# Kernel optimization log

Hardware: AMD Instinct MI355X
Metric: run time of the kernel (lower is better)

## Reference

```python
import jax, jax.numpy as jnp
import numpy as np

NB, DIM, DSTATE, DCONV, EXPAND = 4, 256, 16, 4, 2
DIN = EXPAND * DIM                 # 512
DTRANK = (DIM + 15) // 16          # 16, mamba-ssm default dt_rank = ceil(d_model/16)
B, L = 16, 512


def layer_norm(x, w, b, eps=1e-5):
    mu = x.mean(-1, keepdims=True)
    var = x.var(-1, keepdims=True)
    return (x - mu) * jax.lax.rsqrt(var + eps) * w + b


def selective_scan(u, delta, A, Bm, Cm, D):
    # u, delta: (B,L,DIN); Bm,Cm: (B,L,N); A: (DIN,N); D: (DIN,)
    def step(h, xs):
        d_t, B_t, C_t, u_t = xs          # (B,DIN), (B,N), (B,N), (B,DIN)
        dA = jnp.exp(d_t[..., None] * A)                                  # (B,DIN,N)
        h = dA * h + d_t[..., None] * B_t[:, None, :] * u_t[..., None]   # (B,DIN,N)
        y = jnp.einsum('bdn,bn->bd', h, C_t)
        return h, y

    h0 = jnp.zeros((u.shape[0], u.shape[2], A.shape[1]), u.dtype)
    xs = (delta.transpose(1, 0, 2), Bm.transpose(1, 0, 2),
          Cm.transpose(1, 0, 2), u.transpose(1, 0, 2))
    _, ys = jax.lax.scan(step, h0, xs)
    return ys.transpose(1, 0, 2) + u * D


def mamba_block(x, ln_w, ln_b, in_w, in_b, cw, cb, xp_w, dtw, dtb, A_log, D, ow):
    h = layer_norm(x, ln_w, ln_b)
    xz = h @ in_w.T + in_b                       # (B,L,2*DIN)
    xin, z = xz[..., :DIN], xz[..., DIN:]
    # causal depthwise conv over the sequence dim
    xc = jax.lax.conv_general_dilated(
        xin.transpose(0, 2, 1), cw[:, None, :], (1,), [(DCONV - 1, 0)],
        dimension_numbers=('NCH', 'OIH', 'NCH'), feature_group_count=DIN)
    xc = jax.nn.silu(xc + cb[None, :, None]).transpose(0, 2, 1)   # (B,L,DIN)
    dbc = xc @ xp_w.T                                             # (B,L,DTRANK+2*N)
    dt = jax.nn.softplus(dbc[..., :DTRANK] @ dtw.T + dtb)         # (B,L,DIN)
    Bm = dbc[..., DTRANK:DTRANK + DSTATE]
    Cm = dbc[..., DTRANK + DSTATE:]
    y = selective_scan(xc, dt, -jnp.exp(A_log), Bm, Cm, D)
    return x + (y * jax.nn.silu(z)) @ ow.T       # dropout = identity at eval


def setup_inputs() -> dict:
    key = jax.random.key(0)
    ks = jax.random.split(key, 8)
    s = 0.02
    A_log = jnp.tile(jnp.log(jnp.arange(1, DSTATE + 1, dtype=jnp.float32))[None, None, :],
                     (NB, DIN, 1))
    return {
        'x': jax.random.normal(ks[0], (B, L, DIM), jnp.float32),
        'ln_w': jnp.ones((NB, DIM), jnp.float32),
        'ln_b': jnp.zeros((NB, DIM), jnp.float32),
        'in_proj_w': jax.random.normal(ks[1], (NB, 2 * DIN, DIM), jnp.float32) * s,
        'in_proj_b': jnp.zeros((NB, 2 * DIN), jnp.float32),
        'conv_w': jax.random.normal(ks[2], (NB, DIN, DCONV), jnp.float32) * s,
        'conv_b': jnp.zeros((NB, DIN), jnp.float32),
        'x_proj_w': jax.random.normal(ks[3], (NB, DTRANK + 2 * DSTATE, DIN), jnp.float32) * s,
        'dt_proj_w': jax.random.normal(ks[4], (NB, DIN, DTRANK), jnp.float32) * s,
        'dt_proj_b': jax.random.uniform(ks[5], (NB, DIN), jnp.float32, -4.0, -3.0),
        'A_log': A_log,
        'D': jnp.ones((NB, DIN), jnp.float32),
        'out_proj_w': jax.random.normal(ks[6], (NB, DIM, DIN), jnp.float32) * s,
    }


def reference(x, ln_w, ln_b, in_proj_w, in_proj_b, conv_w, conv_b, x_proj_w,
              dt_proj_w, dt_proj_b, A_log, D, out_proj_w):
    for i in range(NB):
        x = mamba_block(x, ln_w[i], ln_b[i], in_proj_w[i], in_proj_b[i],
                        conv_w[i], conv_b[i], x_proj_w[i], dt_proj_w[i],
                        dt_proj_b[i], A_log[i], D[i], out_proj_w[i])
    return x
```

## Files before the change

### kernel.cpp

```cpp
#include <hip/hip_runtime.h>
#include <math.h>

#define NB 4
#define DIMM 256
#define DSTATE 16
#define DCONV 4
#define DIN 512
#define DTRANK 16
#define BB 16
#define LL 512
#define TT (BB * LL)
#define XZ_DIM (2 * DIN)
#define DBC_DIM (DTRANK + 2 * DSTATE)
#define NC 32
#define CHUNK (LL / NC)

__device__ __forceinline__ unsigned short f2bf(float f) {
    union { float f; unsigned int u; } v; v.f = f;
    unsigned int r = v.u + 0x7fff + ((v.u >> 16) & 1);
    return (unsigned short)(r >> 16);
}
__device__ __forceinline__ float bf2f(unsigned short u) {
    union { unsigned int i; float f; } v; v.i = ((unsigned int)u) << 16;
    return v.f;
}

__global__ __launch_bounds__(256) void cvt3_kernel(const float* __restrict__ s1,
                                                   unsigned short* __restrict__ d1, int n1,
                                                   const float* __restrict__ s2,
                                                   unsigned short* __restrict__ d2, int n2,
                                                   const float* __restrict__ s3,
                                                   unsigned short* __restrict__ d3, int n3) {
    int stride = gridDim.x * 256;
    for (int i = blockIdx.x * 256 + threadIdx.x; i < n1; i += stride) {
        float4 v = ((const float4*)s1)[i];
        ushort4 o; o.x = f2bf(v.x); o.y = f2bf(v.y); o.z = f2bf(v.z); o.w = f2bf(v.w);
        ((ushort4*)d1)[i] = o;
    }
    for (int i = blockIdx.x * 256 + threadIdx.x; i < n2; i += stride) {
        float4 v = ((const float4*)s2)[i];
        ushort4 o; o.x = f2bf(v.x); o.y = f2bf(v.y); o.z = f2bf(v.z); o.w = f2bf(v.w);
        ((ushort4*)d2)[i] = o;
    }
    for (int i = blockIdx.x * 256 + threadIdx.x; i < n3; i += stride) {
        float4 v = ((const float4*)s3)[i];
        ushort4 o; o.x = f2bf(v.x); o.y = f2bf(v.y); o.z = f2bf(v.z); o.w = f2bf(v.w);
        ((ushort4*)d3)[i] = o;
    }
}

__global__ __launch_bounds__(256) void ln_kernel(const float* __restrict__ x,
                                                 const float* __restrict__ w,
                                                 const float* __restrict__ bvec,
                                                 unsigned short* __restrict__ out) {
    int t = blockIdx.x;
    int i = threadIdx.x;
    float v = x[t * DIMM + i];
    float s = v, s2 = v * v;
#pragma unroll
    for (int off = 1; off < 64; off <<= 1) {
        s  += __shfl_xor(s, off);
        s2 += __shfl_xor(s2, off);
    }
    __shared__ float ss[4], ss2[4];
    int wid = i >> 6;
    if ((i & 63) == 0) { ss[wid] = s; ss2[wid] = s2; }
    __syncthreads();
    s  = ss[0] + ss[1] + ss[2] + ss[3];
    s2 = ss2[0] + ss2[1] + ss2[2] + ss2[3];
    float mu  = s * (1.0f / DIMM);
    float var = s2 * (1.0f / DIMM) - mu * mu;
    float r   = rsqrtf(var + 1e-5f);
    out[t * DIMM + i] = f2bf((v - mu) * r * w[i] + bvec[i]);
}

#define GBM2 128
#define GBN2 128
#define GBK2 32
#define LDW2 (GBK2 + 8)
__global__ __launch_bounds__(256) void gemm128(const unsigned short* __restrict__ A, int lda,
                                               const unsigned short* __restrict__ Bw, int ldb,
                                               const float* __restrict__ bias,
                                               unsigned short* __restrict__ C1b,
                                               unsigned short* __restrict__ C2b, int nsplit,
                                               int ldc, int K) {
    using short8  = __attribute__((ext_vector_type(8))) short;
    using floatx4 = __attribute__((ext_vector_type(4))) float;
    __shared__ __align__(16) unsigned short As[GBM2 * LDW2];
    __shared__ __align__(16) unsigned short Bs[GBN2 * LDW2];

    int tid  = threadIdx.x;
    int m0   = blockIdx.y * GBM2;
    int n0   = blockIdx.x * GBN2;
    int w    = tid >> 6;
    int lane = tid & 63;
    int wm   = (w & 1) * 64;
    int wn   = (w >> 1) * 64;
    int lr   = lane & 15;
    int quad = lane >> 4;

    floatx4 acc[4][4] = {};

    int ar = tid >> 1;
    int ak = (tid & 1) * 16;

    for (int k0 = 0; k0 < K; k0 += GBK2) {
        {
            const unsigned short* src = &A[(size_t)(m0 + ar) * lda + k0 + ak];
            int4 a0 = *(const int4*)(src);
            int4 a1 = *(const int4*)(src + 8);
            *(int4*)&As[ar * LDW2 + ak]     = a0;
            *(int4*)&As[ar * LDW2 + ak + 8] = a1;
        }
        {
            const unsigned short* src = &Bw[(size_t)(n0 + ar) * ldb + k0 + ak];
            int4 b0 = *(const int4*)(src);
            int4 b1 = *(const int4*)(src + 8);
            *(int4*)&Bs[ar * LDW2 + ak]     = b0;
            *(int4*)&Bs[ar * LDW2 + ak + 8] = b1;
        }
        __syncthreads();
        short8 af[4], bf[4];
#pragma unroll
        for (int i = 0; i < 4; ++i)
            af[i] = *(const short8*)&As[(wm + i * 16 + lr) * LDW2 + quad * 8];
#pragma unroll
        for (int j = 0; j < 4; ++j)
            bf[j] = *(const short8*)&Bs[(wn + j * 16 + lr) * LDW2 + quad * 8];
#pragma unroll
        for (int i = 0; i < 4; ++i)
#pragma unroll
            for (int j = 0; j < 4; ++j)
                acc[i][j] = __builtin_amdgcn_mfma_f32_16x16x32_bf16(af[i], bf[j], acc[i][j], 0, 0, 0);
        __syncthreads();
    }

#pragma unroll
    for (int j = 0; j < 4; ++j) {
        int cn = n0 + wn + j * 16 + lr;
        float bb = bias ? bias[cn] : 0.0f;
        unsigned short* dst = (cn < nsplit) ? C1b : C2b;
        int col = (cn < nsplit) ? cn : cn - nsplit;
#pragma unroll
        for (int i = 0; i < 4; ++i)
#pragma unroll
            for (int r = 0; r < 4; ++r) {
                int cm = m0 + wm + i * 16 + quad * 4 + r;
                dst[(size_t)cm * ldc + col] = f2bf(acc[i][j][r] + bb);
            }
    }
}

#define TBM 128
#define TBN 64
#define TBK 32
#define LDKW (TBK + 8)
__global__ __launch_bounds__(256) void gemm_bf16(const unsigned short* __restrict__ A, int lda,
                                                 const unsigned short* __restrict__ Bw, int ldb,
                                                 const float* __restrict__ bias,
                                                 const float* __restrict__ resid,
                                                 float* __restrict__ C,
                                                 unsigned short* __restrict__ C1b,
                                                 unsigned short* __restrict__ C2b, int nsplit,
                                                 int ldc, int N, int K) {
    using short8  = __attribute__((ext_vector_type(8))) short;
    using floatx4 = __attribute__((ext_vector_type(4))) float;
    __shared__ __align__(16) unsigned short As[TBM * LDKW];
    __shared__ __align__(16) unsigned short Bs[TBN * LDKW];

    int tid  = threadIdx.x;
    int m0   = blockIdx.y * TBM;
    int n0   = blockIdx.x * TBN;
    int w    = tid >> 6;
    int lane = tid & 63;
    int wm   = (w & 1) * 64;
    int wn   = (w >> 1) * 32;
    int lr   = lane & 15;
    int quad = lane >> 4;

    floatx4 acc[4][2] = {};

    int ar = tid >> 1;
    int ak = (tid & 1) * 16;
    int br = tid >> 2;
    int bk = (tid & 3) * 8;

    for (int k0 = 0; k0 < K; k0 += TBK) {
        {
            const unsigned short* src = &A[(size_t)(m0 + ar) * lda + k0 + ak];
            int4 a0 = *(const int4*)(src);
            int4 a1 = *(const int4*)(src + 8);
            *(int4*)&As[ar * LDKW + ak]     = a0;
            *(int4*)&As[ar * LDKW + ak + 8] = a1;
        }
        {
            int gn = n0 + br;
            int4 b0 = make_int4(0, 0, 0, 0);
            if (gn < N) b0 = *(const int4*)&Bw[(size_t)gn * ldb + k0 + bk];
            *(int4*)&Bs[br * LDKW + bk] = b0;
        }
        __syncthreads();
        short8 af[4], bf[2];
#pragma unroll
        for (int i = 0; i < 4; ++i)
            af[i] = *(const short8*)&As[(wm + i * 16 + lr) * LDKW + quad * 8];
#pragma unroll
        for (int j = 0; j < 2; ++j)
            bf[j] = *(const short8*)&Bs[(wn + j * 16 + lr) * LDKW + quad * 8];
#pragma unroll
        for (int i = 0; i < 4; ++i)
#pragma unroll
            for (int j = 0; j < 2; ++j)
                acc[i][j] = __builtin_amdgcn_mfma_f32_16x16x32_bf16(af[i], bf[j], acc[i][j], 0, 0, 0);
        __syncthreads();
    }

#pragma unroll
    for (int j = 0; j < 2; ++j) {
        int cn = n0 + wn + j * 16 + lr;
        if (cn < N) {
            float bb = bias ? bias[cn] : 0.0f;
            if (C1b) {
                unsigned short* dst = (cn < nsplit) ? C1b : C2b;
                int col = (cn < nsplit) ? cn : cn - nsplit;
#pragma unroll
                for (int i = 0; i < 4; ++i)
#pragma unroll
                    for (int r = 0; r < 4; ++r) {
                        int cm = m0 + wm + i * 16 + quad * 4 + r;
                        dst[(size_t)cm * ldc + col] = f2bf(acc[i][j][r] + bb);
                    }
            } else {
#pragma unroll
                for (int i = 0; i < 4; ++i)
#pragma unroll
                    for (int r = 0; r < 4; ++r) {
                        int cm = m0 + wm + i * 16 + quad * 4 + r;
                        float v = acc[i][j][r] + bb;
                        if (resid) v += resid[(size_t)cm * ldc + cn];
                        C[(size_t)cm * ldc + cn] = v;
                    }
            }
        }
    }
}

__global__ __launch_bounds__(256) void conv_silu(const unsigned short* __restrict__ Xb,
                                                 const float* __restrict__ cw,
                                                 const float* __restrict__ cb,
                                                 unsigned short* __restrict__ xcb) {
    int idx = blockIdx.x * blockDim.x + threadIdx.x;
    int d = idx & (DIN - 1);
    int t = idx >> 9;
    int l = t & (LL - 1);
    int bq = t >> 9;
    float acc = cb[d];
#pragma unroll
    for (int k = 0; k < DCONV; ++k) {
        int ls = l - (DCONV - 1) + k;
        if (ls >= 0) acc += cw[d * DCONV + k] * bf2f(Xb[(size_t)(bq * LL + ls) * DIN + d]);
    }
    float v = acc / (1.0f + __expf(-acc));
    xcb[(size_t)t * DIN + d] = f2bf(v);
}

__global__ __launch_bounds__(256) void dt_kernel(const float* __restrict__ dbc,
                                                 const float* __restrict__ dtw,
                                                 const float* __restrict__ dtbias,
                                                 unsigned short* __restrict__ dtout) {
    int idx = blockIdx.x * blockDim.x + threadIdx.x;
    int d = idx & (DIN - 1);
    int t = idx >> 9;
    float a = dtbias[d];
    const float4* wv = (const float4*)(dtw + d * DTRANK);
    const float* dr = dbc + (size_t)t * DBC_DIM;
#pragma unroll
    for (int q = 0; q < 4; ++q) {
        float4 w4 = wv[q];
        a += w4.x * dr[q * 4 + 0] + w4.y * dr[q * 4 + 1] +
             w4.z * dr[q * 4 + 2] + w4.w * dr[q * 4 + 3];
    }
    float sp = (a > 20.0f) ? a : log1pf(__expf(a));
    dtout[(size_t)t * DIN + d] = f2bf(sp);
}

__global__ __launch_bounds__(256) void scan_p1(const unsigned short* __restrict__ xcb,
                                               const unsigned short* __restrict__ dtb,
                                               const float* __restrict__ dbc,
                                               const float* __restrict__ A_log,
                                               float* __restrict__ S,
                                               float* __restrict__ H) {
    int bid = blockIdx.x;
    int dq = bid & 3;
    int c  = (bid >> 2) & (NC - 1);
    int b  = bid >> 7;
    int dloc = threadIdx.x >> 1;
    int sh   = threadIdx.x & 1;
    int d  = dq * 128 + dloc;
    int n0 = sh * 8;
    int base = b * LL + c * CHUNK;

    __shared__ float LB[CHUNK * DBC_DIM];
    for (int i = threadIdx.x; i < CHUNK * DBC_DIM / 4; i += 256)
        ((float4*)LB)[i] = ((const float4*)(dbc + (size_t)base * DBC_DIM))[i];

    float a[8];
    {
        const float4* ar = (const float4*)(A_log + d * DSTATE + n0);
        float4 v0 = ar[0], v1 = ar[1];
        a[0] = -__expf(v0.x); a[1] = -__expf(v0.y); a[2] = -__expf(v0.z); a[3] = -__expf(v0.w);
        a[4] = -__expf(v1.x); a[5] = -__expf(v1.y); a[6] = -__expf(v1.z); a[7] = -__expf(v1.w);
    }
    __syncthreads();

    float h[8];
#pragma unroll
    for (int j = 0; j < 8; ++j) h[j] = 0.0f;
    float Ssum = 0.0f;
    float u   = bf2f(xcb[(size_t)base * DIN + d]);
    float dtv = bf2f(dtb[(size_t)base * DIN + d]);
#pragma unroll 4
    for (int s = 0; s < CHUNK; ++s) {
        float nu  = bf2f(xcb[(size_t)(base + s + 1) * DIN + d]);
        float ndt = bf2f(dtb[(size_t)(base + s + 1) * DIN + d]);
        const float* row = &LB[s * DBC_DIM];
        float4 b0 = *(const float4*)&row[DTRANK + n0];
        float4 b1 = *(const float4*)&row[DTRANK + n0 + 4];
        const float btv[8] = {b0.x, b0.y, b0.z, b0.w, b1.x, b1.y, b1.z, b1.w};
        Ssum += dtv;
        float wv = dtv * u;
#pragma unroll
        for (int j = 0; j < 8; ++j) {
            float dA = __expf(dtv * a[j]);
            h[j] = dA * h[j] + wv * btv[j];
        }
        u = nu; dtv = ndt;
    }
    size_t sc = (size_t)b * NC + c;
    if (sh == 0) S[sc * DIN + d] = Ssum;
#pragma unroll
    for (int j = 0; j < 8; ++j) H[(sc * DIN + d) * 16 + n0 + j] = h[j];
}

__global__ __launch_bounds__(256) void scan_p2(const float* __restrict__ A_log,
                                               const float* __restrict__ S,
                                               float* __restrict__ H) {
    int idx = blockIdx.x * 256 + threadIdx.x;
    int n = idx & 15;
    int d = (idx >> 4) & (DIN - 1);
    int b = idx >> 13;
    float a = -__expf(A_log[d * DSTATE + n]);
    float h = 0.0f;
#pragma unroll
    for (int c = 0; c < NC; ++c) {
        size_t sc = (size_t)b * NC + c;
        float Sv = S[sc * DIN + d];
        size_t q = (sc * DIN + d) * 16 + n;
        float Hc = H[q];
        H[q] = h;
        h = __expf(a * Sv) * h + Hc;
    }
}

__global__ __launch_bounds__(256) void scan_p3(const unsigned short* __restrict__ xcb,
                                               const unsigned short* __restrict__ dtb,
                                               const unsigned short* __restrict__ Zb,
                                               const float* __restrict__ dbc,
                                               const float* __restrict__ A_log,
                                               const float* __restrict__ Dp,
                                               const float* __restrict__ Hin,
                                               unsigned short* __restrict__ gb) {
    int bid = blockIdx.x;
    int dq = bid & 3;
    int c  = (bid >> 2) & (NC - 1);
    int b  = bid >> 7;
    int dloc = threadIdx.x >> 1;
    int sh   = threadIdx.x & 1;
    int d  = dq * 128 + dloc;
    int n0 = sh * 8;
    int base = b * LL + c * CHUNK;

    __shared__ float LB[CHUNK * DBC_DIM];
    for (int i = threadIdx.x; i < CHUNK * DBC_DIM / 4; i += 256)
        ((float4*)LB)[i] = ((const float4*)(dbc + (size_t)base * DBC_DIM))[i];

    float a[8];
    {
        const float4* ar = (const float4*)(A_log + d * DSTATE + n0);
        float4 v0 = ar[0], v1 = ar[1];
        a[0] = -__expf(v0.x); a[1] = -__expf(v0.y); a[2] = -__expf(v0.z); a[3] = -__expf(v0.w);
        a[4] = -__expf(v1.x); a[5] = -__expf(v1.y); a[6] = -__expf(v1.z); a[7] = -__expf(v1.w);
    }
    float Dd = Dp[d];
    size_t sc = (size_t)b * NC + c;
    float h[8];
#pragma unroll
    for (int j = 0; j < 8; ++j) h[j] = Hin[(sc * DIN + d) * 16 + n0 + j];
    __syncthreads();

    float u   = bf2f(xcb[(size_t)base * DIN + d]);
    float dtv = bf2f(dtb[(size_t)base * DIN + d]);
#pragma unroll 4
    for (int s = 0; s < CHUNK; ++s) {
        float nu  = bf2f(xcb[(size_t)(base + s + 1) * DIN + d]);
        float ndt = bf2f(dtb[(size_t)(base + s + 1) * DIN + d]);
        const float* row = &LB[s * DBC_DIM];
        float4 b0 = *(const float4*)&row[DTRANK + n0];
        float4 b1 = *(const float4*)&row[DTRANK + n0 + 4];
        float4 c0 = *(const float4*)&row[DTRANK + DSTATE + n0];
        float4 c1 = *(const float4*)&row[DTRANK + DSTATE + n0 + 4];
        const float btv[8] = {b0.x, b0.y, b0.z, b0.w, b1.x, b1.y, b1.z, b1.w};
        const float ctv[8] = {c0.x, c0.y, c0.z, c0.w, c1.x, c1.y, c1.z, c1.w};
        float wv = dtv * u;
        float y  = (sh == 0) ? u * Dd : 0.0f;
#pragma unroll
        for (int j = 0; j < 8; ++j) {
            float dA = __expf(dtv * a[j]);
            h[j] = dA * h[j] + wv * btv[j];
            y += h[j] * ctv[j];
        }
        y += __shfl_xor(y, 1);
        if (sh == 0) {
            float zf = bf2f(Zb[(size_t)(base + s) * DIN + d]);
            float g = y * (zf / (1.0f + __expf(-zf)));
            gb[(size_t)(base + s) * DIN + d] = f2bf(g);
        }
        u = nu; dtv = ndt;
    }
}

extern "C" void kernel_launch(void* const* d_in, const int* in_sizes, int n_in,
                              void* d_out, int out_size, void* d_ws, size_t ws_size,
                              hipStream_t stream) {
    const float* x_in   = (const float*)d_in[0];
    const float* ln_w   = (const float*)d_in[1];
    const float* ln_b   = (const float*)d_in[2];
    const float* in_w   = (const float*)d_in[3];
    const float* in_b   = (const float*)d_in[4];
    const float* conv_w = (const float*)d_in[5];
    const float* conv_b = (const float*)d_in[6];
    const float* xp_w   = (const float*)d_in[7];
    const float* dt_w   = (const float*)d_in[8];
    const float* dt_b   = (const float*)d_in[9];
    const float* A_log  = (const float*)d_in[10];
    const float* Dp     = (const float*)d_in[11];
    const float* ow     = (const float*)d_in[12];
    float* out = (float*)d_out;

    const size_t M = 1048576;
    float* ws = (float*)d_ws;
    float* xbuf = ws;
    unsigned short* hb  = (unsigned short*)(ws + 2 * M);
    float* dbc = ws + 3 * M;
    unsigned short* Xb  = (unsigned short*)(ws + 4 * M);
    unsigned short* Zb  = (unsigned short*)(ws + 6 * M);
    unsigned short* xcb = (unsigned short*)(ws + 8 * M);
    unsigned short* dtb = (unsigned short*)(ws + 10 * M);
    unsigned short* gb  = (unsigned short*)(ws + 12 * M);
    float* Hbuf = ws + 14 * M;
    float* Sbuf = ws + 18 * M;
    unsigned short* inwb = (unsigned short*)(ws + 18 * M + 262144);
    unsigned short* owb  = inwb + (size_t)NB * XZ_DIM * DIMM;
    unsigned short* xpwb = owb + (size_t)NB * DIMM * DIN;

    cvt3_kernel<<<256, 256, 0, stream>>>(
        in_w, inwb, NB * XZ_DIM * DIMM / 4,
        ow,   owb,  NB * DIMM * DIN / 4,
        xp_w, xpwb, NB * DBC_DIM * DIN / 4);

    for (int layer = 0; layer < NB; ++layer) {
        const float* xi = (layer == 0) ? x_in : xbuf;
        float* xo = (layer == NB - 1) ? out : xbuf;

        ln_kernel<<<TT, 256, 0, stream>>>(xi, ln_w + layer * DIMM, ln_b + layer * DIMM, hb);

        gemm128<<<dim3(XZ_DIM / GBN2, TT / GBM2), 256, 0, stream>>>(
            hb, DIMM, inwb + (size_t)layer * XZ_DIM * DIMM, DIMM,
            in_b + layer * XZ_DIM, Xb, Zb, DIN, DIN, DIMM);

        conv_silu<<<(TT * DIN) / 256, 256, 0, stream>>>(
            Xb, conv_w + layer * DIN * DCONV, conv_b + layer * DIN, xcb);

        gemm_bf16<<<dim3(1, TT / TBM), 256, 0, stream>>>(
            xcb, DIN, xpwb + (size_t)layer * DBC_DIM * DIN, DIN,
            nullptr, nullptr, dbc, nullptr, nullptr, 0, DBC_DIM, DBC_DIM, DIN);

        dt_kernel<<<(TT * DIN) / 256, 256, 0, stream>>>(
            dbc, dt_w + (size_t)layer * DIN * DTRANK, dt_b + layer * DIN, dtb);

        const float* Al = A_log + (size_t)layer * DIN * DSTATE;
        scan_p1<<<BB * NC * 4, 256, 0, stream>>>(xcb, dtb, dbc, Al, Sbuf, Hbuf);
        scan_p2<<<(BB * DIN * 16) / 256, 256, 0, stream>>>(Al, Sbuf, Hbuf);
        scan_p3<<<BB * NC * 4, 256, 0, stream>>>(xcb, dtb, Zb, dbc, Al,
                                                 Dp + layer * DIN, Hbuf, gb);

        gemm_bf16<<<dim3(DIMM / TBN, TT / TBM), 256, 0, stream>>>(
            gb, DIN, owb + (size_t)layer * DIMM * DIN, DIN,
            nullptr, xi, xo, nullptr, nullptr, 0, DIMM, DIMM, DIN);
    }
}
```

Before: 681.8 us.

## Fuse layernorm into in_proj GEMM and conv+x_proj+dt_proj into one kernel

```diff
diff --git a/kernel.cpp b/kernel.cpp
--- a/kernel.cpp
+++ b/kernel.cpp
@@ -49,45 +49,23 @@
     }
 }
 
-__global__ __launch_bounds__(256) void ln_kernel(const float* __restrict__ x,
-                                                 const float* __restrict__ w,
-                                                 const float* __restrict__ bvec,
-                                                 unsigned short* __restrict__ out) {
-    int t = blockIdx.x;
-    int i = threadIdx.x;
-    float v = x[t * DIMM + i];
-    float s = v, s2 = v * v;
-#pragma unroll
-    for (int off = 1; off < 64; off <<= 1) {
-        s  += __shfl_xor(s, off);
-        s2 += __shfl_xor(s2, off);
-    }
-    __shared__ float ss[4], ss2[4];
-    int wid = i >> 6;
-    if ((i & 63) == 0) { ss[wid] = s; ss2[wid] = s2; }
-    __syncthreads();
-    s  = ss[0] + ss[1] + ss[2] + ss[3];
-    s2 = ss2[0] + ss2[1] + ss2[2] + ss2[3];
-    float mu  = s * (1.0f / DIMM);
-    float var = s2 * (1.0f / DIMM) - mu * mu;
-    float r   = rsqrtf(var + 1e-5f);
-    out[t * DIMM + i] = f2bf((v - mu) * r * w[i] + bvec[i]);
-}
-
 #define GBM2 128
 #define GBN2 128
 #define GBK2 32
 #define LDW2 (GBK2 + 8)
-__global__ __launch_bounds__(256) void gemm128(const unsigned short* __restrict__ A, int lda,
-                                               const unsigned short* __restrict__ Bw, int ldb,
-                                               const float* __restrict__ bias,
-                                               unsigned short* __restrict__ C1b,
-                                               unsigned short* __restrict__ C2b, int nsplit,
-                                               int ldc, int K) {
+__global__ __launch_bounds__(256) void ln_inproj(const float* __restrict__ x,
+                                                 const float* __restrict__ lnw,
+                                                 const float* __restrict__ lnb,
+                                                 const unsigned short* __restrict__ Bw,
+                                                 const float* __restrict__ bias,
+                                                 unsigned short* __restrict__ C1b,
+                                                 unsigned short* __restrict__ C2b,
+                                                 int nsplit, int ldc) {
     using short8  = __attribute__((ext_vector_type(8))) short;
     using floatx4 = __attribute__((ext_vector_type(4))) float;
     __shared__ __align__(16) unsigned short As[GBM2 * LDW2];
     __shared__ __align__(16) unsigned short Bs[GBN2 * LDW2];
+    __shared__ float muS[GBM2], rsS[GBM2], lwS[DIMM], lbS[DIMM];
 
     int tid  = threadIdx.x;
     int m0   = blockIdx.y * GBM2;
@@ -99,21 +77,54 @@
     int lr   = lane & 15;
     int quad = lane >> 4;
 
+    {
+        int r = tid >> 1;
+        int seg = (tid & 1) * 128;
+        const float4* xr = (const float4*)(x + (size_t)(m0 + r) * DIMM + seg);
+        float s = 0.0f, s2 = 0.0f;
+#pragma unroll
+        for (int i = 0; i < 32; ++i) {
+            float4 v = xr[i];
+            s  += v.x + v.y + v.z + v.w;
+            s2 += v.x * v.x + v.y * v.y + v.z * v.z + v.w * v.w;
+        }
+        s  += __shfl_xor(s, 1);
+        s2 += __shfl_xor(s2, 1);
+        if ((tid & 1) == 0) {
+            float mu  = s * (1.0f / DIMM);
+            float var = s2 * (1.0f / DIMM) - mu * mu;
+            muS[r] = mu;
+            rsS[r] = rsqrtf(var + 1e-5f);
+        }
+        lwS[tid] = lnw[tid];
+        lbS[tid] = lnb[tid];
+    }
+    __syncthreads();
+
     floatx4 acc[4][4] = {};
 
     int ar = tid >> 1;
     int ak = (tid & 1) * 16;
 
-    for (int k0 = 0; k0 < K; k0 += GBK2) {
+    for (int k0 = 0; k0 < DIMM; k0 += GBK2) {
         {
-            const unsigned short* src = &A[(size_t)(m0 + ar) * lda + k0 + ak];
-            int4 a0 = *(const int4*)(src);
-            int4 a1 = *(const int4*)(src + 8);
-            *(int4*)&As[ar * LDW2 + ak]     = a0;
-            *(int4*)&As[ar * LDW2 + ak + 8] = a1;
+            float mu = muS[ar], rs = rsS[ar];
+            const float4* src = (const float4*)(x + (size_t)(m0 + ar) * DIMM + k0 + ak);
+            unsigned short tmp[16];
+#pragma unroll
+            for (int q = 0; q < 4; ++q) {
+                float4 v = src[q];
+                int kk = k0 + ak + q * 4;
+                tmp[q * 4 + 0] = f2bf((v.x - mu) * rs * lwS[kk + 0] + lbS[kk + 0]);
+                tmp[q * 4 + 1] = f2bf((v.y - mu) * rs * lwS[kk + 1] + lbS[kk + 1]);
+                tmp[q * 4 + 2] = f2bf((v.z - mu) * rs * lwS[kk + 2] + lbS[kk + 2]);
+                tmp[q * 4 + 3] = f2bf((v.w - mu) * rs * lwS[kk + 3] + lbS[kk + 3]);
+            }
+            *(int4*)&As[ar * LDW2 + ak]     = *(const int4*)&tmp[0];
+            *(int4*)&As[ar * LDW2 + ak + 8] = *(const int4*)&tmp[8];
         }
         {
-            const unsigned short* src = &Bw[(size_t)(n0 + ar) * ldb + k0 + ak];
+            const unsigned short* src = &Bw[(size_t)(n0 + ar) * DIMM + k0 + ak];
             int4 b0 = *(const int4*)(src);
             int4 b1 = *(const int4*)(src + 8);
             *(int4*)&Bs[ar * LDW2 + ak]     = b0;
@@ -138,7 +149,7 @@
 #pragma unroll
     for (int j = 0; j < 4; ++j) {
         int cn = n0 + wn + j * 16 + lr;
-        float bb = bias ? bias[cn] : 0.0f;
+        float bb = bias[cn];
         unsigned short* dst = (cn < nsplit) ? C1b : C2b;
         int col = (cn < nsplit) ? cn : cn - nsplit;
 #pragma unroll
@@ -148,6 +159,115 @@
                 int cm = m0 + wm + i * 16 + quad * 4 + r;
                 dst[(size_t)cm * ldc + col] = f2bf(acc[i][j][r] + bb);
             }
+    }
+}
+
+#define CXM 64
+__global__ __launch_bounds__(256) void conv_xp(const unsigned short* __restrict__ Xb,
+                                               const float* __restrict__ cw,
+                                               const float* __restrict__ cb,
+                                               const unsigned short* __restrict__ xpw,
+                                               const float* __restrict__ dtw,
+                                               const float* __restrict__ dtbias,
+                                               unsigned short* __restrict__ xcb,
+                                               float* __restrict__ dbc,
+                                               unsigned short* __restrict__ dtout) {
+    using short8  = __attribute__((ext_vector_type(8))) short;
+    using floatx4 = __attribute__((ext_vector_type(4))) float;
+    __shared__ __align__(16) unsigned short As[CXM * LDW2];
+    __shared__ __align__(16) unsigned short Bs[48 * LDW2];
+    __shared__ float dbcS[CXM * DBC_DIM];
+
+    int t0 = blockIdx.x * CXM;
+    int bq = t0 >> 9;
+    int l0 = t0 & (LL - 1);
+    int tid  = threadIdx.x;
+    int w    = tid >> 6;
+    int lane = tid & 63;
+    int lr   = lane & 15;
+    int quad = lane >> 4;
+    int wm   = w * 16;
+
+    int ch = tid & 31;
+    int tg = tid >> 5;
+    int br = tid >> 2;
+    int bk = (tid & 3) * 8;
+
+    floatx4 acc[3] = {};
+
+    for (int k0 = 0; k0 < DIN; k0 += 32) {
+        int d = k0 + ch;
+        float4 cwv = *(const float4*)&cw[d * DCONV];
+        float cbv = cb[d];
+        const float cwk[4] = {cwv.x, cwv.y, cwv.z, cwv.w};
+#pragma unroll
+        for (int tt = 0; tt < 8; ++tt) {
+            int l = l0 + tg * 8 + tt;
+            int t = t0 + tg * 8 + tt;
+            float a0 = cbv;
+#pragma unroll
+            for (int k = 0; k < DCONV; ++k) {
+                int ls = l - (DCONV - 1) + k;
+                if (ls >= 0) a0 += cwk[k] * bf2f(Xb[(size_t)(bq * LL + ls) * DIN + d]);
+            }
+            float v = a0 / (1.0f + __expf(-a0));
+            unsigned short bv = f2bf(v);
+            As[(tg * 8 + tt) * LDW2 + ch] = bv;
+            xcb[(size_t)t * DIN + d] = bv;
+        }
+        if (br < 48) {
+            int4 b0 = *(const int4*)&xpw[(size_t)br * DIN + k0 + bk];
+            *(int4*)&Bs[br * LDW2 + bk] = b0;
+        }
+        __syncthreads();
+        short8 af = *(const short8*)&As[(wm + lr) * LDW2 + quad * 8];
+#pragma unroll
+        for (int j = 0; j < 3; ++j) {
+            short8 bf = *(const short8*)&Bs[(j * 16 + lr) * LDW2 + quad * 8];
+            acc[j] = __builtin_amdgcn_mfma_f32_16x16x32_bf16(af, bf, acc[j], 0, 0, 0);
+        }
+        __syncthreads();
+    }
+
+#pragma unroll
+    for (int j = 0; j < 3; ++j) {
+        int col = j * 16 + lr;
+#pragma unroll
+        for (int r = 0; r < 4; ++r) {
+            int row = wm + quad * 4 + r;
+            float v = acc[j][r];
+            dbcS[row * DBC_DIM + col] = v;
+            dbc[(size_t)(t0 + row) * DBC_DIM + col] = v;
+        }
+    }
+    __syncthreads();
+
+    {
+        int d0 = tid * 2;
+        float wa[16], wb[16];
+        const float4* wra = (const float4*)(dtw + d0 * DTRANK);
+        const float4* wrb = (const float4*)(dtw + (d0 + 1) * DTRANK);
+#pragma unroll
+        for (int q = 0; q < 4; ++q) {
+            float4 va = wra[q], vb = wrb[q];
+            wa[q * 4 + 0] = va.x; wa[q * 4 + 1] = va.y; wa[q * 4 + 2] = va.z; wa[q * 4 + 3] = va.w;
+            wb[q * 4 + 0] = vb.x; wb[q * 4 + 1] = vb.y; wb[q * 4 + 2] = vb.z; wb[q * 4 + 3] = vb.w;
+        }
+        float ba = dtbias[d0], bb = dtbias[d0 + 1];
+        for (int tt = 0; tt < CXM; ++tt) {
+            const float* row = &dbcS[tt * DBC_DIM];
+            float da = ba, db = bb;
+#pragma unroll
+            for (int q = 0; q < 4; ++q) {
+                float4 rv = *(const float4*)&row[q * 4];
+                da += rv.x * wa[q*4+0] + rv.y * wa[q*4+1] + rv.z * wa[q*4+2] + rv.w * wa[q*4+3];
+                db += rv.x * wb[q*4+0] + rv.y * wb[q*4+1] + rv.z * wb[q*4+2] + rv.w * wb[q*4+3];
+            }
+            float sa = (da > 20.0f) ? da : log1pf(__expf(da));
+            float sb = (db > 20.0f) ? db : log1pf(__expf(db));
+            unsigned int packed = (unsigned int)f2bf(sa) | ((unsigned int)f2bf(sb) << 16);
+            *(unsigned int*)&dtout[(size_t)(t0 + tt) * DIN + d0] = packed;
+        }
     }
 }
 
@@ -243,45 +363,6 @@
             }
         }
     }
-}
-
-__global__ __launch_bounds__(256) void conv_silu(const unsigned short* __restrict__ Xb,
-                                                 const float* __restrict__ cw,
-                                                 const float* __restrict__ cb,
-                                                 unsigned short* __restrict__ xcb) {
-    int idx = blockIdx.x * blockDim.x + threadIdx.x;
-    int d = idx & (DIN - 1);
-    int t = idx >> 9;
-    int l = t & (LL - 1);
-    int bq = t >> 9;
-    float acc = cb[d];
-#pragma unroll
-    for (int k = 0; k < DCONV; ++k) {
-        int ls = l - (DCONV - 1) + k;
-        if (ls >= 0) acc += cw[d * DCONV + k] * bf2f(Xb[(size_t)(bq * LL + ls) * DIN + d]);
-    }
-    float v = acc / (1.0f + __expf(-acc));
-    xcb[(size_t)t * DIN + d] = f2bf(v);
-}
-
-__global__ __launch_bounds__(256) void dt_kernel(const float* __restrict__ dbc,
-                                                 const float* __restrict__ dtw,
-                                                 const float* __restrict__ dtbias,
-                                                 unsigned short* __restrict__ dtout) {
-    int idx = blockIdx.x * blockDim.x + threadIdx.x;
-    int d = idx & (DIN - 1);
-    int t = idx >> 9;
-    float a = dtbias[d];
-    const float4* wv = (const float4*)(dtw + d * DTRANK);
-    const float* dr = dbc + (size_t)t * DBC_DIM;
-#pragma unroll
-    for (int q = 0; q < 4; ++q) {
-        float4 w4 = wv[q];
-        a += w4.x * dr[q * 4 + 0] + w4.y * dr[q * 4 + 1] +
-             w4.z * dr[q * 4 + 2] + w4.w * dr[q * 4 + 3];
-    }
-    float sp = (a > 20.0f) ? a : log1pf(__expf(a));
-    dtout[(size_t)t * DIN + d] = f2bf(sp);
 }
 
 __global__ __launch_bounds__(256) void scan_p1(const unsigned short* __restrict__ xcb,
@@ -450,7 +531,6 @@
     const size_t M = 1048576;
     float* ws = (float*)d_ws;
     float* xbuf = ws;
-    unsigned short* hb  = (unsigned short*)(ws + 2 * M);
     float* dbc = ws + 3 * M;
     unsigned short* Xb  = (unsigned short*)(ws + 4 * M);
     unsigned short* Zb  = (unsigned short*)(ws + 6 * M);
@@ -472,21 +552,16 @@
         const float* xi = (layer == 0) ? x_in : xbuf;
         float* xo = (layer == NB - 1) ? out : xbuf;
 
-        ln_kernel<<<TT, 256, 0, stream>>>(xi, ln_w + layer * DIMM, ln_b + layer * DIMM, hb);
-
-        gemm128<<<dim3(XZ_DIM / GBN2, TT / GBM2), 256, 0, stream>>>(
-            hb, DIMM, inwb + (size_t)layer * XZ_DIM * DIMM, DIMM,
-            in_b + layer * XZ_DIM, Xb, Zb, DIN, DIN, DIMM);
-
-        conv_silu<<<(TT * DIN) / 256, 256, 0, stream>>>(
-            Xb, conv_w + layer * DIN * DCONV, conv_b + layer * DIN, xcb);
-
-        gemm_bf16<<<dim3(1, TT / TBM), 256, 0, stream>>>(
-            xcb, DIN, xpwb + (size_t)layer * DBC_DIM * DIN, DIN,
-            nullptr, nullptr, dbc, nullptr, nullptr, 0, DBC_DIM, DBC_DIM, DIN);
-
-        dt_kernel<<<(TT * DIN) / 256, 256, 0, stream>>>(
-            dbc, dt_w + (size_t)layer * DIN * DTRANK, dt_b + layer * DIN, dtb);
+        ln_inproj<<<dim3(XZ_DIM / GBN2, TT / GBM2), 256, 0, stream>>>(
+            xi, ln_w + layer * DIMM, ln_b + layer * DIMM,
+            inwb + (size_t)layer * XZ_DIM * DIMM, in_b + layer * XZ_DIM,
+            Xb, Zb, DIN, DIN);
+
+        conv_xp<<<TT / CXM, 256, 0, stream>>>(
+            Xb, conv_w + layer * DIN * DCONV, conv_b + layer * DIN,
+            xpwb + (size_t)layer * DBC_DIM * DIN,
+            dt_w + (size_t)layer * DIN * DTRANK, dt_b + layer * DIN,
+            xcb, dbc, dtb);
 
         const float* Al = A_log + (size_t)layer * DIN * DSTATE;
         scan_p1<<<BB * NC * 4, 256, 0, stream>>>(xcb, dtb, dbc, Al, Sbuf, Hbuf);
```

New measurement: 807.8 us. +18.5%, slower.

## Fuse layernorm into in-proj GEMM and merge scan phases into cooperative kernel

Applied to the files above, without the earlier changes.

```diff
diff --git a/kernel.cpp b/kernel.cpp
--- a/kernel.cpp
+++ b/kernel.cpp
@@ -1,5 +1,8 @@
 #include <hip/hip_runtime.h>
+#include <hip/hip_cooperative_groups.h>
 #include <math.h>
+
+namespace cg = cooperative_groups;
 
 #define NB 4
 #define DIMM 256
@@ -49,45 +52,23 @@
     }
 }
 
-__global__ __launch_bounds__(256) void ln_kernel(const float* __restrict__ x,
-                                                 const float* __restrict__ w,
-                                                 const float* __restrict__ bvec,
-                                                 unsigned short* __restrict__ out) {
-    int t = blockIdx.x;
-    int i = threadIdx.x;
-    float v = x[t * DIMM + i];
-    float s = v, s2 = v * v;
-#pragma unroll
-    for (int off = 1; off < 64; off <<= 1) {
-        s  += __shfl_xor(s, off);
-        s2 += __shfl_xor(s2, off);
-    }
-    __shared__ float ss[4], ss2[4];
-    int wid = i >> 6;
-    if ((i & 63) == 0) { ss[wid] = s; ss2[wid] = s2; }
-    __syncthreads();
-    s  = ss[0] + ss[1] + ss[2] + ss[3];
-    s2 = ss2[0] + ss2[1] + ss2[2] + ss2[3];
-    float mu  = s * (1.0f / DIMM);
-    float var = s2 * (1.0f / DIMM) - mu * mu;
-    float r   = rsqrtf(var + 1e-5f);
-    out[t * DIMM + i] = f2bf((v - mu) * r * w[i] + bvec[i]);
-}
-
 #define GBM2 128
 #define GBN2 128
 #define GBK2 32
 #define LDW2 (GBK2 + 8)
-__global__ __launch_bounds__(256) void gemm128(const unsigned short* __restrict__ A, int lda,
-                                               const unsigned short* __restrict__ Bw, int ldb,
-                                               const float* __restrict__ bias,
-                                               unsigned short* __restrict__ C1b,
-                                               unsigned short* __restrict__ C2b, int nsplit,
-                                               int ldc, int K) {
+__global__ __launch_bounds__(256) void ln_inproj(const float* __restrict__ x,
+                                                 const float* __restrict__ lnw,
+                                                 const float* __restrict__ lnb,
+                                                 const unsigned short* __restrict__ Bw,
+                                                 const float* __restrict__ bias,
+                                                 unsigned short* __restrict__ C1b,
+                                                 unsigned short* __restrict__ C2b,
+                                                 int nsplit, int ldc) {
     using short8  = __attribute__((ext_vector_type(8))) short;
     using floatx4 = __attribute__((ext_vector_type(4))) float;
     __shared__ __align__(16) unsigned short As[GBM2 * LDW2];
     __shared__ __align__(16) unsigned short Bs[GBN2 * LDW2];
+    __shared__ float muS[GBM2], rsS[GBM2], lwS[DIMM], lbS[DIMM];
 
     int tid  = threadIdx.x;
     int m0   = blockIdx.y * GBM2;
@@ -99,21 +80,54 @@
     int lr   = lane & 15;
     int quad = lane >> 4;
 
+    {
+        int r = tid >> 1;
+        int seg = (tid & 1) * 128;
+        const float4* xr = (const float4*)(x + (size_t)(m0 + r) * DIMM + seg);
+        float s = 0.0f, s2 = 0.0f;
+#pragma unroll
+        for (int i = 0; i < 32; ++i) {
+            float4 v = xr[i];
+            s  += v.x + v.y + v.z + v.w;
+            s2 += v.x * v.x + v.y * v.y + v.z * v.z + v.w * v.w;
+        }
+        s  += __shfl_xor(s, 1);
+        s2 += __shfl_xor(s2, 1);
+        if ((tid & 1) == 0) {
+            float mu  = s * (1.0f / DIMM);
+            float var = s2 * (1.0f / DIMM) - mu * mu;
+            muS[r] = mu;
+            rsS[r] = rsqrtf(var + 1e-5f);
+        }
+        lwS[tid] = lnw[tid];
+        lbS[tid] = lnb[tid];
+    }
+    __syncthreads();
+
     floatx4 acc[4][4] = {};
 
     int ar = tid >> 1;
     int ak = (tid & 1) * 16;
 
-    for (int k0 = 0; k0 < K; k0 += GBK2) {
+    for (int k0 = 0; k0 < DIMM; k0 += GBK2) {
         {
-            const unsigned short* src = &A[(size_t)(m0 + ar) * lda + k0 + ak];
-            int4 a0 = *(const int4*)(src);
-            int4 a1 = *(const int4*)(src + 8);
-            *(int4*)&As[ar * LDW2 + ak]     = a0;
-            *(int4*)&As[ar * LDW2 + ak + 8] = a1;
+            float mu = muS[ar], rs = rsS[ar];
+            const float4* src = (const float4*)(x + (size_t)(m0 + ar) * DIMM + k0 + ak);
+            unsigned short tmp[16];
+#pragma unroll
+            for (int q = 0; q < 4; ++q) {
+                float4 v = src[q];
+                int kk = k0 + ak + q * 4;
+                tmp[q * 4 + 0] = f2bf((v.x - mu) * rs * lwS[kk + 0] + lbS[kk + 0]);
+                tmp[q * 4 + 1] = f2bf((v.y - mu) * rs * lwS[kk + 1] + lbS[kk + 1]);
+                tmp[q * 4 + 2] = f2bf((v.z - mu) * rs * lwS[kk + 2] + lbS[kk + 2]);
+                tmp[q * 4 + 3] = f2bf((v.w - mu) * rs * lwS[kk + 3] + lbS[kk + 3]);
+            }
+            *(int4*)&As[ar * LDW2 + ak]     = *(const int4*)&tmp[0];
+            *(int4*)&As[ar * LDW2 + ak + 8] = *(const int4*)&tmp[8];
         }
         {
-            const unsigned short* src = &Bw[(size_t)(n0 + ar) * ldb + k0 + ak];
+            const unsigned short* src = &Bw[(size_t)(n0 + ar) * DIMM + k0 + ak];
             int4 b0 = *(const int4*)(src);
             int4 b1 = *(const int4*)(src + 8);
             *(int4*)&Bs[ar * LDW2 + ak]     = b0;
@@ -138,7 +152,7 @@
 #pragma unroll
     for (int j = 0; j < 4; ++j) {
         int cn = n0 + wn + j * 16 + lr;
-        float bb = bias ? bias[cn] : 0.0f;
+        float bb = bias[cn];
         unsigned short* dst = (cn < nsplit) ? C1b : C2b;
         int col = (cn < nsplit) ? cn : cn - nsplit;
 #pragma unroll
@@ -284,25 +298,26 @@
     dtout[(size_t)t * DIN + d] = f2bf(sp);
 }
 
-__global__ __launch_bounds__(256) void scan_p1(const unsigned short* __restrict__ xcb,
-                                               const unsigned short* __restrict__ dtb,
-                                               const float* __restrict__ dbc,
-                                               const float* __restrict__ A_log,
-                                               float* __restrict__ S,
-                                               float* __restrict__ H) {
-    int bid = blockIdx.x;
-    int dq = bid & 3;
-    int c  = (bid >> 2) & (NC - 1);
-    int b  = bid >> 7;
+__global__ __launch_bounds__(256, 4) void scan_coop(const unsigned short* __restrict__ xcb,
+                                                    const unsigned short* __restrict__ dtb,
+                                                    const unsigned short* __restrict__ Zb,
+                                                    const float* __restrict__ dbc,
+                                                    const float* __restrict__ A_log,
+                                                    const float* __restrict__ Dp,
+                                                    float* __restrict__ S,
+                                                    float* __restrict__ H,
+                                                    unsigned short* __restrict__ gb) {
+    cg::grid_group gg = cg::this_grid();
+    __shared__ float LB[CHUNK * DBC_DIM];
+
+    int rb = blockIdx.x;
+    int dq = rb & 3;
+    int ch = (rb >> 2) & 15;
+    int b  = rb >> 6;
     int dloc = threadIdx.x >> 1;
     int sh   = threadIdx.x & 1;
     int d  = dq * 128 + dloc;
     int n0 = sh * 8;
-    int base = b * LL + c * CHUNK;
-
-    __shared__ float LB[CHUNK * DBC_DIM];
-    for (int i = threadIdx.x; i < CHUNK * DBC_DIM / 4; i += 256)
-        ((float4*)LB)[i] = ((const float4*)(dbc + (size_t)base * DBC_DIM))[i];
 
     float a[8];
     {
@@ -311,121 +326,111 @@
         a[0] = -__expf(v0.x); a[1] = -__expf(v0.y); a[2] = -__expf(v0.z); a[3] = -__expf(v0.w);
         a[4] = -__expf(v1.x); a[5] = -__expf(v1.y); a[6] = -__expf(v1.z); a[7] = -__expf(v1.w);
     }
-    __syncthreads();
-
-    float h[8];
-#pragma unroll
-    for (int j = 0; j < 8; ++j) h[j] = 0.0f;
-    float Ssum = 0.0f;
-    float u   = bf2f(xcb[(size_t)base * DIN + d]);
-    float dtv = bf2f(dtb[(size_t)base * DIN + d]);
+
+#pragma unroll
+    for (int r = 0; r < 2; ++r) {
+        int c = ch * 2 + r;
+        int base = b * LL + c * CHUNK;
+        __syncthreads();
+        for (int i = threadIdx.x; i < CHUNK * DBC_DIM / 4; i += 256)
+            ((float4*)LB)[i] = ((const float4*)(dbc + (size_t)base * DBC_DIM))[i];
+        __syncthreads();
+
+        float h[8];
+#pragma unroll
+        for (int j = 0; j < 8; ++j) h[j] = 0.0f;
+        float Ssum = 0.0f;
+        float u   = bf2f(xcb[(size_t)base * DIN + d]);
+        float dtv = bf2f(dtb[(size_t)base * DIN + d]);
 #pragma unroll 4
-    for (int s = 0; s < CHUNK; ++s) {
-        float nu  = bf2f(xcb[(size_t)(base + s + 1) * DIN + d]);
-        float ndt = bf2f(dtb[(size_t)(base + s + 1) * DIN + d]);
-        const float* row = &LB[s * DBC_DIM];
-        float4 b0 = *(const float4*)&row[DTRANK + n0];
-        float4 b1 = *(const float4*)&row[DTRANK + n0 + 4];
-        const float btv[8] = {b0.x, b0.y, b0.z, b0.w, b1.x, b1.y, b1.z, b1.w};
-        Ssum += dtv;
-        float wv = dtv * u;
-#pragma unroll
-        for (int j = 0; j < 8; ++j) {
-            float dA = __expf(dtv * a[j]);
-            h[j] = dA * h[j] + wv * btv[j];
-        }
-        u = nu; dtv = ndt;
-    }
-    size_t sc = (size_t)b * NC + c;
-    if (sh == 0) S[sc * DIN + d] = Ssum;
-#pragma unroll
-    for (int j = 0; j < 8; ++j) H[(sc * DIN + d) * 16 + n0 + j] = h[j];
-}
-
-__global__ __launch_bounds__(256) void scan_p2(const float* __restrict__ A_log,
-                                               const float* __restrict__ S,
-                                               float* __restrict__ H) {
-    int idx = blockIdx.x * 256 + threadIdx.x;
-    int n = idx & 15;
-    int d = (idx >> 4) & (DIN - 1);
-    int b = idx >> 13;
-    float a = -__expf(A_log[d * DSTATE + n]);
-    float h = 0.0f;
-#pragma unroll
-    for (int c = 0; c < NC; ++c) {
+        for (int s = 0; s < CHUNK; ++s) {
+            float nu  = bf2f(xcb[(size_t)(base + s + 1) * DIN + d]);
+            float ndt = bf2f(dtb[(size_t)(base + s + 1) * DIN + d]);
+            const float* row = &LB[s * DBC_DIM];
+            float4 b0 = *(const float4*)&row[DTRANK + n0];
+            float4 b1 = *(const float4*)&row[DTRANK + n0 + 4];
+            const float btv[8] = {b0.x, b0.y, b0.z, b0.w, b1.x, b1.y, b1.z, b1.w};
+            Ssum += dtv;
+            float wv = dtv * u;
+#pragma unroll
+            for (int j = 0; j < 8; ++j) {
+                float dA = __expf(dtv * a[j]);
+                h[j] = dA * h[j] + wv * btv[j];
+            }
+            u = nu; dtv = ndt;
+        }
         size_t sc = (size_t)b * NC + c;
-        float Sv = S[sc * DIN + d];
-        size_t q = (sc * DIN + d) * 16 + n;
-        float Hc = H[q];
-        H[q] = h;
-        h = __expf(a * Sv) * h + Hc;
-    }
-}
-
-__global__ __launch_bounds__(256) void scan_p3(const unsigned short* __restrict__ xcb,
-                                               const unsigned short* __restrict__ dtb,
-                                               const unsigned short* __restrict__ Zb,
-                                               const float* __restrict__ dbc,
-                                               const float* __restrict__ A_log,
-                                               const float* __restrict__ Dp,
-                                               const float* __restrict__ Hin,
-                                               unsigned short* __restrict__ gb) {
-    int bid = blockIdx.x;
-    int dq = bid & 3;
-    int c  = (bid >> 2) & (NC - 1);
-    int b  = bid >> 7;
-    int dloc = threadIdx.x >> 1;
-    int sh   = threadIdx.x & 1;
-    int d  = dq * 128 + dloc;
-    int n0 = sh * 8;
-    int base = b * LL + c * CHUNK;
-
-    __shared__ float LB[CHUNK * DBC_DIM];
-    for (int i = threadIdx.x; i < CHUNK * DBC_DIM / 4; i += 256)
-        ((float4*)LB)[i] = ((const float4*)(dbc + (size_t)base * DBC_DIM))[i];
-
-    float a[8];
-    {
-        const float4* ar = (const float4*)(A_log + d * DSTATE + n0);
-        float4 v0 = ar[0], v1 = ar[1];
-        a[0] = -__expf(v0.x); a[1] = -__expf(v0.y); a[2] = -__expf(v0.z); a[3] = -__expf(v0.w);
-        a[4] = -__expf(v1.x); a[5] = -__expf(v1.y); a[6] = -__expf(v1.z); a[7] = -__expf(v1.w);
-    }
+        if (sh == 0) S[sc * DIN + d] = Ssum;
+#pragma unroll
+        for (int j = 0; j < 8; ++j) H[(sc * DIN + d) * 16 + n0 + j] = h[j];
+    }
+
+    gg.sync();
+
+    if (rb < 512) {
+        int idx = rb * 256 + threadIdx.x;
+        int n2 = idx & 15;
+        int d2 = (idx >> 4) & (DIN - 1);
+        int b2 = idx >> 13;
+        float a2 = -__expf(A_log[d2 * DSTATE + n2]);
+        float h2 = 0.0f;
+#pragma unroll
+        for (int c = 0; c < NC; ++c) {
+            size_t sc = (size_t)b2 * NC + c;
+            float Sv = S[sc * DIN + d2];
+            size_t q = (sc * DIN + d2) * 16 + n2;
+            float Hc = H[q];
+            H[q] = h2;
+            h2 = __expf(a2 * Sv) * h2 + Hc;
+        }
+    }
+
+    gg.sync();
+
     float Dd = Dp[d];
-    size_t sc = (size_t)b * NC + c;
-    float h[8];
-#pragma unroll
-    for (int j = 0; j < 8; ++j) h[j] = Hin[(sc * DIN + d) * 16 + n0 + j];
-    __syncthreads();
-
-    float u   = bf2f(xcb[(size_t)base * DIN + d]);
-    float dtv = bf2f(dtb[(size_t)base * DIN + d]);
+#pragma unroll
+    for (int r = 0; r < 2; ++r) {
+        int c = ch * 2 + r;
+        int base = b * LL + c * CHUNK;
+        size_t sc = (size_t)b * NC + c;
+        __syncthreads();
+        for (int i = threadIdx.x; i < CHUNK * DBC_DIM / 4; i += 256)
+            ((float4*)LB)[i] = ((const float4*)(dbc + (size_t)base * DBC_DIM))[i];
+        __syncthreads();
+
+        float h[8];
+#pragma unroll
+        for (int j = 0; j < 8; ++j) h[j] = H[(sc * DIN + d) * 16 + n0 + j];
+
+        float u   = bf2f(xcb[(size_t)base * DIN + d]);
+        float dtv = bf2f(dtb[(size_t)base * DIN + d]);
 #pragma unroll 4
-    for (int s = 0; s < CHUNK; ++s) {
-        float nu  = bf2f(xcb[(size_t)(base + s + 1) * DIN + d]);
-        float ndt = bf2f(dtb[(size_t)(base + s + 1) * DIN + d]);
-        const float* row = &LB[s * DBC_DIM];
-        float4 b0 = *(const float4*)&row[DTRANK + n0];
-        float4 b1 = *(const float4*)&row[DTRANK + n0 + 4];
-        float4 c0 = *(const float4*)&row[DTRANK + DSTATE + n0];
-        float4 c1 = *(const float4*)&row[DTRANK + DSTATE + n0 + 4];
-        const float btv[8] = {b0.x, b0.y, b0.z, b0.w, b1.x, b1.y, b1.z, b1.w};
-        const float ctv[8] = {c0.x, c0.y, c0.z, c0.w, c1.x, c1.y, c1.z, c1.w};
-        float wv = dtv * u;
-        float y  = (sh == 0) ? u * Dd : 0.0f;
-#pragma unroll
-        for (int j = 0; j < 8; ++j) {
-            float dA = __expf(dtv * a[j]);
-            h[j] = dA * h[j] + wv * btv[j];
-            y += h[j] * ctv[j];
-        }
-        y += __shfl_xor(y, 1);
-        if (sh == 0) {
-            float zf = bf2f(Zb[(size_t)(base + s) * DIN + d]);
-            float g = y * (zf / (1.0f + __expf(-zf)));
-            gb[(size_t)(base + s) * DIN + d] = f2bf(g);
-        }
-        u = nu; dtv = ndt;
+        for (int s = 0; s < CHUNK; ++s) {
+            float nu  = bf2f(xcb[(size_t)(base + s + 1) * DIN + d]);
+            float ndt = bf2f(dtb[(size_t)(base + s + 1) * DIN + d]);
+            const float* row = &LB[s * DBC_DIM];
+            float4 b0 = *(const float4*)&row[DTRANK + n0];
+            float4 b1 = *(const float4*)&row[DTRANK + n0 + 4];
+            float4 c0 = *(const float4*)&row[DTRANK + DSTATE + n0];
+            float4 c1 = *(const float4*)&row[DTRANK + DSTATE + n0 + 4];
+            const float btv[8] = {b0.x, b0.y, b0.z, b0.w, b1.x, b1.y, b1.z, b1.w};
+            const float ctv[8] = {c0.x, c0.y, c0.z, c0.w, c1.x, c1.y, c1.z, c1.w};
+            float wv = dtv * u;
+            float y  = (sh == 0) ? u * Dd : 0.0f;
+#pragma unroll
+            for (int j = 0; j < 8; ++j) {
+                float dA = __expf(dtv * a[j]);
+                h[j] = dA * h[j] + wv * btv[j];
+                y += h[j] * ctv[j];
+            }
+            y += __shfl_xor(y, 1);
+            if (sh == 0) {
+                float zf = bf2f(Zb[(size_t)(base + s) * DIN + d]);
+                float g = y * (zf / (1.0f + __expf(-zf)));
+                gb[(size_t)(base + s) * DIN + d] = f2bf(g);
+            }
+            u = nu; dtv = ndt;
+        }
     }
 }
 
@@ -450,7 +455,6 @@
     const size_t M = 1048576;
     float* ws = (float*)d_ws;
     float* xbuf = ws;
-    unsigned short* hb  = (unsigned short*)(ws + 2 * M);
     float* dbc = ws + 3 * M;
     unsigned short* Xb  = (unsigned short*)(ws + 4 * M);
     unsigned short* Zb  = (unsigned short*)(ws + 6 * M);
@@ -472,11 +476,10 @@
         const float* xi = (layer == 0) ? x_in : xbuf;
         float* xo = (layer == NB - 1) ? out : xbuf;
 
-        ln_kernel<<<TT, 256, 0, stream>>>(xi, ln_w + layer * DIMM, ln_b + layer * DIMM, hb);
-
-        gemm128<<<dim3(XZ_DIM / GBN2, TT / GBM2), 256, 0, stream>>>(
-            hb, DIMM, inwb + (size_t)layer * XZ_DIM * DIMM, DIMM,
-            in_b + layer * XZ_DIM, Xb, Zb, DIN, DIN, DIMM);
+        ln_inproj<<<dim3(XZ_DIM / GBN2, TT / GBM2), 256, 0, stream>>>(
+            xi, ln_w + layer * DIMM, ln_b + layer * DIMM,
+            inwb + (size_t)layer * XZ_DIM * DIMM, in_b + layer * XZ_DIM,
+            Xb, Zb, DIN, DIN);
 
         conv_silu<<<(TT * DIN) / 256, 256, 0, stream>>>(
             Xb, conv_w + layer * DIN * DCONV, conv_b + layer * DIN, xcb);
@@ -488,11 +491,22 @@
         dt_kernel<<<(TT * DIN) / 256, 256, 0, stream>>>(
             dbc, dt_w + (size_t)layer * DIN * DTRANK, dt_b + layer * DIN, dtb);
 
-        const float* Al = A_log + (size_t)layer * DIN * DSTATE;
-        scan_p1<<<BB * NC * 4, 256, 0, stream>>>(xcb, dtb, dbc, Al, Sbuf, Hbuf);
-        scan_p2<<<(BB * DIN * 16) / 256, 256, 0, stream>>>(Al, Sbuf, Hbuf);
-        scan_p3<<<BB * NC * 4, 256, 0, stream>>>(xcb, dtb, Zb, dbc, Al,
-                                                 Dp + layer * DIN, Hbuf, gb);
+        {
+            const unsigned short* xcb_c = xcb;
+            const unsigned short* dtb_c = dtb;
+            const unsigned short* Zb_c  = Zb;
+            const float* dbc_c = dbc;
+            const float* Al  = A_log + (size_t)layer * DIN * DSTATE;
+            const float* Dpl = Dp + layer * DIN;
+            float* S_c = Sbuf;
+            float* H_c = Hbuf;
+            unsigned short* gb_c = gb;
+            void* kargs[] = {(void*)&xcb_c, (void*)&dtb_c, (void*)&Zb_c,
+                             (void*)&dbc_c, (void*)&Al, (void*)&Dpl,
+                             (void*)&S_c, (void*)&H_c, (void*)&gb_c};
+            hipLaunchCooperativeKernel((const void*)scan_coop, dim3(1024), dim3(256),
+                                       kargs, 0, stream);
+        }
 
         gemm_bf16<<<dim3(DIMM / TBN, TT / TBM), 256, 0, stream>>>(
             gb, DIN, owb + (size_t)layer * DIMM * DIN, DIN,
```

New measurement: 1.799 ms. 164% more time.

## Fold inter-chunk state propagation into scan_p3, removing scan_p2 launch

Applied to the files above, without the earlier changes.

```diff
diff --git a/kernel.cpp b/kernel.cpp
--- a/kernel.cpp
+++ b/kernel.cpp
@@ -342,33 +342,14 @@
     for (int j = 0; j < 8; ++j) H[(sc * DIN + d) * 16 + n0 + j] = h[j];
 }
 
-__global__ __launch_bounds__(256) void scan_p2(const float* __restrict__ A_log,
-                                               const float* __restrict__ S,
-                                               float* __restrict__ H) {
-    int idx = blockIdx.x * 256 + threadIdx.x;
-    int n = idx & 15;
-    int d = (idx >> 4) & (DIN - 1);
-    int b = idx >> 13;
-    float a = -__expf(A_log[d * DSTATE + n]);
-    float h = 0.0f;
-#pragma unroll
-    for (int c = 0; c < NC; ++c) {
-        size_t sc = (size_t)b * NC + c;
-        float Sv = S[sc * DIN + d];
-        size_t q = (sc * DIN + d) * 16 + n;
-        float Hc = H[q];
-        H[q] = h;
-        h = __expf(a * Sv) * h + Hc;
-    }
-}
-
 __global__ __launch_bounds__(256) void scan_p3(const unsigned short* __restrict__ xcb,
                                                const unsigned short* __restrict__ dtb,
                                                const unsigned short* __restrict__ Zb,
                                                const float* __restrict__ dbc,
                                                const float* __restrict__ A_log,
                                                const float* __restrict__ Dp,
-                                               const float* __restrict__ Hin,
+                                               const float* __restrict__ S,
+                                               const float* __restrict__ H,
                                                unsigned short* __restrict__ gb) {
     int bid = blockIdx.x;
     int dq = bid & 3;
@@ -392,10 +373,21 @@
         a[4] = -__expf(v1.x); a[5] = -__expf(v1.y); a[6] = -__expf(v1.z); a[7] = -__expf(v1.w);
     }
     float Dd = Dp[d];
-    size_t sc = (size_t)b * NC + c;
+
     float h[8];
 #pragma unroll
-    for (int j = 0; j < 8; ++j) h[j] = Hin[(sc * DIN + d) * 16 + n0 + j];
+    for (int j = 0; j < 8; ++j) h[j] = 0.0f;
+    for (int cp = 0; cp < c; ++cp) {
+        size_t scp = (size_t)b * NC + cp;
+        float Sv = S[scp * DIN + d];
+        const float* hp = &H[(scp * DIN + d) * 16 + n0];
+        float4 h0 = *(const float4*)(hp);
+        float4 h1 = *(const float4*)(hp + 4);
+        const float hv[8] = {h0.x, h0.y, h0.z, h0.w, h1.x, h1.y, h1.z, h1.w};
+#pragma unroll
+        for (int j = 0; j < 8; ++j)
+            h[j] = __expf(a[j] * Sv) * h[j] + hv[j];
+    }
     __syncthreads();
 
     float u   = bf2f(xcb[(size_t)base * DIN + d]);
@@ -490,9 +482,8 @@
 
         const float* Al = A_log + (size_t)layer * DIN * DSTATE;
         scan_p1<<<BB * NC * 4, 256, 0, stream>>>(xcb, dtb, dbc, Al, Sbuf, Hbuf);
-        scan_p2<<<(BB * DIN * 16) / 256, 256, 0, stream>>>(Al, Sbuf, Hbuf);
         scan_p3<<<BB * NC * 4, 256, 0, stream>>>(xcb, dtb, Zb, dbc, Al,
-                                                 Dp + layer * DIN, Hbuf, gb);
+                                                 Dp + layer * DIN, Sbuf, Hbuf, gb);
 
         gemm_bf16<<<dim3(DIMM / TBN, TT / TBM), 256, 0, stream>>>(
             gb, DIN, owb + (size_t)layer * DIMM * DIN, DIN,
```

Result: slower. 733.6 us (+7.6%).
